# Optimization experiments

Hardware: AMD Instinct MI355X
Metric: run time of the kernel (lower is better)

Reference implementation:

```python
import jax, jax.numpy as jnp
import numpy as np

B, T, F, D, H, L, DFF, G = 4, 2048, 512, 1024, 16, 2, 4096, 16
WSCALE = 0.03  # ~1/sqrt(D) so activations stay well-conditioned


def setup_inputs() -> dict:
    key = jax.random.key(0)
    ks = iter(jax.random.split(key, 24))

    def w(shape):
        return jax.random.normal(next(ks), shape, jnp.float32) * WSCALE

    return {
        "x": jax.random.normal(next(ks), (B, T, F), jnp.float32),
        "proj_w": w((D, F)), "proj_b": jnp.zeros((D,), jnp.float32),
        "wq": w((L, D, D)), "wk": w((L, D, D)), "wv": w((L, D, D)),
        "bq": jnp.zeros((L, D), jnp.float32), "bk": jnp.zeros((L, D), jnp.float32), "bv": jnp.zeros((L, D), jnp.float32),
        "wo": w((L, D, D)), "bo": jnp.zeros((L, D), jnp.float32),
        "ln1_g": jnp.ones((L, D), jnp.float32), "ln1_b": jnp.zeros((L, D), jnp.float32),
        "ln2_g": jnp.ones((L, D), jnp.float32), "ln2_b": jnp.zeros((L, D), jnp.float32),
        "w1": w((L, DFF, D)), "b1": jnp.zeros((L, DFF), jnp.float32),
        "w2": w((L, D, DFF)), "b2": jnp.zeros((L, D), jnp.float32),
        "hw1": w((G, D, D)), "hb1": jnp.zeros((G, D), jnp.float32),
        "hw2": w((G, 2, D)), "hb2": jnp.zeros((G, 2), jnp.float32),
        "nhead": H,
    }


def _ln(x, g, b, eps=1e-5):
    m = x.mean(-1, keepdims=True)
    v = ((x - m) ** 2).mean(-1, keepdims=True)
    return (x - m) * jax.lax.rsqrt(v + eps) * g + b


def _pe(t, d):
    # sinusoidal positional encoding, shape (t, d) (d even -> sin/cos interleave)
    pos = jnp.arange(t, dtype=jnp.float32)[:, None]
    div = jnp.exp(jnp.arange(0, d, 2, dtype=jnp.float32) * (-np.log(10000.0) / d))
    ph = pos * div
    return jnp.stack([jnp.sin(ph), jnp.cos(ph)], axis=-1).reshape(t, d)


def reference(x, proj_w, proj_b, wq, wk, wv, bq, bk, bv, wo, bo,
              ln1_g, ln1_b, ln2_g, ln2_b, w1, b1, w2, b2,
              hw1, hb1, hw2, hb2, nhead):
    Bx, Tx, _ = x.shape
    Dm = proj_w.shape[0]
    dh = Dm // nhead
    h = x @ proj_w.T + proj_b + _pe(Tx, Dm)  # (B,T,D)
    for l in range(wq.shape[0]):  # post-norm encoder layers
        q = (h @ wq[l].T + bq[l]).reshape(Bx, Tx, nhead, dh)
        k = (h @ wk[l].T + bk[l]).reshape(Bx, Tx, nhead, dh)
        v = (h @ wv[l].T + bv[l]).reshape(Bx, Tx, nhead, dh)
        # explicit (non-fused) attention path, as forced by need_weights=True
        scores = jnp.einsum('bthd,bshd->bhts', q, k) / jnp.sqrt(jnp.float32(dh))
        attn = jax.nn.softmax(scores, axis=-1)  # (B,H,T,T)
        ctx = jnp.einsum('bhts,bshd->bthd', attn, v).reshape(Bx, Tx, Dm)
        h = _ln(h + ctx @ wo[l].T + bo[l], ln1_g[l], ln1_b[l])
        ff = jax.nn.relu(h @ w1[l].T + b1[l]) @ w2[l].T + b2[l]
        h = _ln(h + ff, ln2_g[l], ln2_b[l])
    hl = h[:, -1, :]  # last-token pooling, (B,D)
    z = jax.nn.relu(jnp.einsum('bd,gkd->bgk', hl, hw1) + hb1)  # per-sector hidden
    logits = jnp.einsum('bgk,gok->bgo', z, hw2) + hb2           # (B,G,2)
    return jax.nn.softmax(logits, axis=-1)
```

## Files before the change

kernel.cpp:

```cpp
#include <hip/hip_runtime.h>
#include <hip/hip_bf16.h>
#include <cstdint>
#include <cstddef>


typedef __bf16 bf16_t;
typedef __attribute__((ext_vector_type(8))) __bf16 bf16x8;
typedef __attribute__((ext_vector_type(4))) __bf16 bf16x4;
typedef __attribute__((ext_vector_type(4))) float f32x4;

#define DEV __device__ __forceinline__
#define AS1 __attribute__((address_space(1)))
#define AS3 __attribute__((address_space(3)))

DEV void gload_lds16(const void* g, void* l) {
  __builtin_amdgcn_global_load_lds((AS1 void*)(g), (AS3 void*)(l), 16, 0, 0);
}

DEV char* swz_ptr(void* base, int row, int colb) {
  return (char*)base + row * 128 + ((((colb >> 4) ^ (row & 7))) << 4) + (colb & 15);
}
DEV const char* swz_ptr(const void* base, int row, int colb) {
  return (const char*)base + row * 128 + ((((colb >> 4) ^ (row & 7))) << 4) +
         (colb & 15);
}

__global__ __launch_bounds__(256) void f2b_kernel(const float* __restrict__ s,
                                                  bf16_t* __restrict__ d, int n4) {
  const int i = blockIdx.x * 256 + threadIdx.x;
  if (i >= n4) return;
  const float4 v = *(const float4*)&s[(size_t)i * 4];
  bf16x4 o = {(bf16_t)v.x, (bf16_t)v.y, (bf16_t)v.z, (bf16_t)v.w};
  *(bf16x4*)&d[(size_t)i * 4] = o;
}

__global__ __launch_bounds__(256) void bcat_kernel(const float* __restrict__ bq,
                                                   const float* __restrict__ bk,
                                                   const float* __restrict__ bv,
                                                   float* __restrict__ out) {
  const int idx = blockIdx.x * 256 + threadIdx.x;
  const int l = idx / 3072, r = idx - l * 3072;
  const int p = r >> 10, i = r & 1023;
  const float* s = (p == 0) ? bq : ((p == 1) ? bk : bv);
  out[idx] = s[l * 1024 + i];
}

__global__ __launch_bounds__(256) void pe_kernel(float* __restrict__ pe) {
  const int idx = blockIdx.x * 256 + threadIdx.x;
  const int t = idx >> 9, i = idx & 511;
  const float dv = __expf((float)(2 * i) * -0.008994473019508785f);
  const float ph = (float)t * dv;
  pe[(size_t)t * 1024 + 2 * i] = sinf(ph);
  pe[(size_t)t * 1024 + 2 * i + 1] = cosf(ph);
}

template <int EPI>
__global__ __launch_bounds__(512, 1) void gemm8(
    const bf16_t* __restrict__ A, const bf16_t* __restrict__ W,
    const float* __restrict__ bias, bf16_t* __restrict__ outb,
    float* __restrict__ outf, const float* __restrict__ res32,
    const float* __restrict__ pe, int M, int N, int K) {
  __shared__ char smem[3][49152];
  const int tid = threadIdx.x, wv = tid >> 6, ln = tid & 63;
  const int nwg = gridDim.x * gridDim.y;
  int bid = blockIdx.y * gridDim.x + blockIdx.x;
  bid = (bid & 7) * (nwg >> 3) + (bid >> 3);
  const int m0 = (bid / gridDim.x) * 256, n0 = (bid % gridDim.x) * 128;
  const int wr = (wv >> 1) * 64, wc = (wv & 1) * 64;
  f32x4 acc[4][4] = {};

  const int tp = tid ^ ((tid >> 3) & 7);
  const int srow = tp >> 3, sc8 = (tp & 7) * 8;
  const bf16_t* pa[4];
  const bf16_t* pb[2];
#pragma unroll
  for (int u = 0; u < 4; ++u) pa[u] = A + (size_t)(m0 + u * 64 + srow) * K + sc8;
#pragma unroll
  for (int u = 0; u < 2; ++u) pb[u] = W + (size_t)(n0 + u * 64 + srow) * K + sc8;
  const int wvb = wv * 1024;

  auto stage = [&](int s) {
    char* bA = &smem[s][0] + wvb;
    char* bB = &smem[s][32768] + wvb;
#pragma unroll
    for (int u = 0; u < 4; ++u) {
      gload_lds16(pa[u], bA + u * 8192);
      pa[u] += 64;
    }
#pragma unroll
    for (int u = 0; u < 2; ++u) {
      gload_lds16(pb[u], bB + u * 8192);
      pb[u] += 64;
    }
  };

  const int NK = K >> 6;
  stage(0);
  stage(1);
  stage(2);
  asm volatile("s_waitcnt vmcnt(12)" ::: "memory");
  __builtin_amdgcn_s_barrier();

  for (int kt = 0; kt < NK; ++kt) {
    const char* bA = &smem[kt % 3][0];
    const char* bB = &smem[kt % 3][32768];
#pragma unroll
    for (int ks = 0; ks < 2; ++ks) {
      const int cb = ks * 64 + (ln >> 4) * 16;
      bf16x8 aF[4], bF[4];
#pragma unroll
      for (int m = 0; m < 4; ++m) {
        const int lb = (wr + m * 16 + (ln & 15)) * 128 + cb;
        aF[m] = *(const bf16x8*)(bA + (lb ^ (((lb >> 7) & 7) << 4)));
      }
#pragma unroll
      for (int n = 0; n < 4; ++n) {
        const int lb = (wc + n * 16 + (ln & 15)) * 128 + cb;
        bF[n] = *(const bf16x8*)(bB + (lb ^ (((lb >> 7) & 7) << 4)));
      }
      __builtin_amdgcn_s_setprio(1);
#pragma unroll
      for (int m = 0; m < 4; ++m)
#pragma unroll
        for (int n = 0; n < 4; ++n)
          acc[m][n] =
              __builtin_amdgcn_mfma_f32_16x16x32_bf16(aF[m], bF[n], acc[m][n], 0, 0, 0);
      __builtin_amdgcn_s_setprio(0);
    }
    __builtin_amdgcn_s_barrier();
    if (kt + 3 < NK) {
      stage(kt % 3);
      asm volatile("s_waitcnt vmcnt(12)" ::: "memory");
    } else if (kt + 2 < NK) {
      asm volatile("s_waitcnt vmcnt(6)" ::: "memory");
    } else {
      asm volatile("s_waitcnt vmcnt(0)" ::: "memory");
    }
    __builtin_amdgcn_s_barrier();
    __builtin_amdgcn_sched_barrier(0);
  }

  const int rr = (ln >> 4) * 4, cc = ln & 15;
#pragma unroll
  for (int m = 0; m < 4; ++m) {
    const int rowb = m0 + wr + m * 16 + rr;
#pragma unroll
    for (int n = 0; n < 4; ++n) {
      const int col = n0 + wc + n * 16 + cc;
      const float bv = bias[col];
#pragma unroll
      for (int r = 0; r < 4; ++r) {
        const int row = rowb + r;
        float v = acc[m][n][r] + bv;
        const size_t o = (size_t)row * N + col;
        if constexpr (EPI == 1) {
          v = fmaxf(v, 0.f);
          outb[o] = (bf16_t)v;
        } else if constexpr (EPI == 2) {
          v += pe[(size_t)(row & 2047) * 1024 + col];
          outb[o] = (bf16_t)v;
          outf[o] = v;
        } else if constexpr (EPI == 3) {
          v += res32[o];
          outf[o] = v;
        } else {
          outb[o] = (bf16_t)v;
        }
      }
    }
  }
}

__global__ __launch_bounds__(256) void ln_kernel(const float* __restrict__ pre,
                                                 const float* __restrict__ g,
                                                 const float* __restrict__ b,
                                                 bf16_t* __restrict__ h16,
                                                 float* __restrict__ h32) {
  const int row = blockIdx.x, tid = threadIdx.x;
  const size_t base = (size_t)row * 1024 + tid * 4;
  const float4 v = *(const float4*)&pre[base];
  float s = v.x + v.y + v.z + v.w;
  float s2 = v.x * v.x + v.y * v.y + v.z * v.z + v.w * v.w;
#pragma unroll
  for (int m = 1; m < 64; m <<= 1) {
    s += __shfl_xor(s, m);
    s2 += __shfl_xor(s2, m);
  }
  __shared__ float ls[4], ls2[4];
  if ((tid & 63) == 0) {
    ls[tid >> 6] = s;
    ls2[tid >> 6] = s2;
  }
  __syncthreads();
  s = ls[0] + ls[1] + ls[2] + ls[3];
  s2 = ls2[0] + ls2[1] + ls2[2] + ls2[3];
  const float mean = s * (1.f / 1024.f);
  const float var = s2 * (1.f / 1024.f) - mean * mean;
  const float rs = rsqrtf(var + 1e-5f);
  const float4 gv = *(const float4*)&g[tid * 4];
  const float4 bv = *(const float4*)&b[tid * 4];
  const float o0 = (v.x - mean) * rs * gv.x + bv.x;
  const float o1 = (v.y - mean) * rs * gv.y + bv.y;
  const float o2 = (v.z - mean) * rs * gv.z + bv.z;
  const float o3 = (v.w - mean) * rs * gv.w + bv.w;
  bf16x4 ob = {(bf16_t)o0, (bf16_t)o1, (bf16_t)o2, (bf16_t)o3};
  *(bf16x4*)&h16[base] = ob;
  float4 of = {o0, o1, o2, o3};
  *(float4*)&h32[base] = of;
}

__global__ __launch_bounds__(256) void transpose_v(const bf16_t* __restrict__ v,
                                                   bf16_t* __restrict__ vt) {
  __shared__ bf16_t tile[64][80];
  const int bh = blockIdx.y, t0 = blockIdx.x * 64;
  const int tid = threadIdx.x;
  const int b = bh >> 4;
  const size_t vbase = ((size_t)(b * 2048 + t0)) * 3072 + (bh & 15) * 64;
#pragma unroll
  for (int p = 0; p < 2; ++p) {
    const int chunk = p * 256 + tid;
    const int tr = chunk >> 3, c8 = (chunk & 7) * 8;
    *(bf16x8*)&tile[tr][c8] = *(const bf16x8*)&v[vbase + (size_t)tr * 3072 + c8];
  }
  __syncthreads();
  const int d = tid >> 2, t8 = (tid & 3) * 16;
  bf16_t tmp[16];
#pragma unroll
  for (int j = 0; j < 16; ++j) tmp[j] = tile[t8 + j][d];
  const size_t obase = ((size_t)bh * 64 + d) * 2048 + t0 + t8;
  *(bf16x8*)&vt[obase] = *(bf16x8*)&tmp[0];
  *(bf16x8*)&vt[obase + 8] = *(bf16x8*)&tmp[8];
}

__global__ __launch_bounds__(256, 2) void attn_kernel(const bf16_t* __restrict__ qkv,
                                                      const bf16_t* __restrict__ vt,
                                                      bf16_t* __restrict__ ctx) {
  constexpr float SCL = 0.18033688011112042f;
  constexpr int QS = 3072;
  __shared__ bf16_t lK[2][64 * 64];
  __shared__ bf16_t lV[2][64 * 64];
  __shared__ bf16_t lP[4][16 * 64];
  const int tid = threadIdx.x, wv = tid >> 6, ln = tid & 63;
  const int nwg = gridDim.x * gridDim.y;
  int bid = blockIdx.y * gridDim.x + blockIdx.x;
  bid = (bid & 7) * (nwg >> 3) + (bid >> 3);
  const int bh = bid / gridDim.x, b = bh >> 4, h = bh & 15;
  const int q0 = (bid % gridDim.x) * 64;
  const int qrow = q0 + wv * 16 + (ln & 15);
  const bf16_t* qp = qkv + (size_t)(b * 2048 + qrow) * QS + h * 64 + (ln >> 4) * 8;
  const bf16x8 aQ0 = *(const bf16x8*)qp;
  const bf16x8 aQ1 = *(const bf16x8*)(qp + 32);
  f32x4 O[4] = {};
  float m_q = -1e30f, l_q = 0.f;
  const int sr = tid >> 3;
  const int scS = ((tid & 7) ^ ((tid >> 3) & 7)) * 8;
  const bf16_t* kp0 = qkv + 1024 + (size_t)(b * 2048 + sr) * QS + h * 64 + scS;
  const bf16_t* kp1 = kp0 + (size_t)32 * QS;
  const bf16_t* vp0 = vt + (size_t)bh * 64 * 2048 + (size_t)sr * 2048 + scS;
  const bf16_t* vp1 = vp0 + 32 * 2048;

  auto stage = [&](int bufi) {
    char* dk = (char*)&lK[bufi][0] + wv * 1024;
    char* dv = (char*)&lV[bufi][0] + wv * 1024;
    gload_lds16(kp0, dk);
    gload_lds16(kp1, dk + 4096);
    gload_lds16(vp0, dv);
    gload_lds16(vp1, dv + 4096);
    kp0 += (size_t)64 * QS;
    kp1 += (size_t)64 * QS;
    vp0 += 64;
    vp1 += 64;
  };

  stage(0);
  asm volatile("s_waitcnt vmcnt(0)" ::: "memory");
  __builtin_amdgcn_s_barrier();

  for (int st = 0; st < 32; ++st) {
    const int cur = st & 1;
    if (st + 1 < 32) stage(cur ^ 1);
    f32x4 sc[4] = {};
    __builtin_amdgcn_s_setprio(1);
#pragma unroll
    for (int ks = 0; ks < 2; ++ks) {
      const int ko = ks * 32 + (ln >> 4) * 8;
      const bf16x8 aQ = ks ? aQ1 : aQ0;
#pragma unroll
      for (int nt = 0; nt < 4; ++nt) {
        const bf16x8 bK = *(const bf16x8*)swz_ptr(&lK[cur][0], nt * 16 + (ln & 15), ko * 2);
        sc[nt] = __builtin_amdgcn_mfma_f32_16x16x32_bf16(bK, aQ, sc[nt], 0, 0, 0);
      }
    }
    __builtin_amdgcn_s_setprio(0);
    float mx = fmaxf(fmaxf(sc[0][0], sc[0][1]), fmaxf(sc[0][2], sc[0][3]));
#pragma unroll
    for (int nt = 1; nt < 4; ++nt)
      mx = fmaxf(mx, fmaxf(fmaxf(sc[nt][0], sc[nt][1]), fmaxf(sc[nt][2], sc[nt][3])));
    mx *= SCL;
    mx = fmaxf(mx, __shfl_xor(mx, 16));
    mx = fmaxf(mx, __shfl_xor(mx, 32));
    if (__any(mx > m_q + 8.f)) {
      const float mnew = fmaxf(m_q, mx);
      const float alpha = exp2f(m_q - mnew);
      m_q = mnew;
      l_q *= alpha;
      float ar[4];
#pragma unroll
      for (int r = 0; r < 4; ++r) ar[r] = __shfl(alpha, (ln >> 4) * 4 + r);
#pragma unroll
      for (int dt = 0; dt < 4; ++dt)
#pragma unroll
        for (int r = 0; r < 4; ++r) O[dt][r] *= ar[r];
    }
    float rs = 0.f;
#pragma unroll
    for (int nt = 0; nt < 4; ++nt) {
      bf16x4 pb;
#pragma unroll
      for (int r = 0; r < 4; ++r) {
        const float p = exp2f(sc[nt][r] * SCL - m_q);
        rs += p;
        pb[r] = (bf16_t)p;
      }
      *(bf16x4*)swz_ptr(&lP[wv][0], ln & 15, nt * 32 + (ln >> 4) * 8) = pb;
    }
    rs += __shfl_xor(rs, 16);
    rs += __shfl_xor(rs, 32);
    l_q += rs;
    __builtin_amdgcn_s_setprio(1);
#pragma unroll
    for (int ks = 0; ks < 2; ++ks) {
      const int ko = ks * 32 + (ln >> 4) * 8;
      const bf16x8 aP = *(const bf16x8*)swz_ptr(&lP[wv][0], ln & 15, ko * 2);
#pragma unroll
      for (int dt = 0; dt < 4; ++dt) {
        const bf16x8 bV = *(const bf16x8*)swz_ptr(&lV[cur][0], dt * 16 + (ln & 15), ko * 2);
        O[dt] = __builtin_amdgcn_mfma_f32_16x16x32_bf16(aP, bV, O[dt], 0, 0, 0);
      }
    }
    __builtin_amdgcn_s_setprio(0);
    asm volatile("s_waitcnt vmcnt(0)" ::: "memory");
    __builtin_amdgcn_s_barrier();
    __builtin_amdgcn_sched_barrier(0);
  }
  const float invl = 1.f / l_q;
  float ir[4];
#pragma unroll
  for (int r = 0; r < 4; ++r) ir[r] = __shfl(invl, (ln >> 4) * 4 + r);
  const int orow = b * 2048 + q0 + wv * 16 + (ln >> 4) * 4;
#pragma unroll
  for (int r = 0; r < 4; ++r) {
#pragma unroll
    for (int dt = 0; dt < 4; ++dt)
      ctx[((size_t)(orow + r)) * 1024 + h * 64 + dt * 16 + (ln & 15)] =
          (bf16_t)(O[dt][r] * ir[r]);
  }
}

__global__ __launch_bounds__(256) void head_z(const float* __restrict__ h32,
                                              const float* __restrict__ hw1,
                                              const float* __restrict__ hb1,
                                              float* __restrict__ z) {
  const int g = blockIdx.x, slab = blockIdx.y;
  const int wv = threadIdx.x >> 6, ln = threadIdx.x & 63;
  float4 hl[4][4];
#pragma unroll
  for (int b = 0; b < 4; ++b)
#pragma unroll
    for (int c = 0; c < 4; ++c)
      hl[b][c] = *(const float4*)&h32[((size_t)b * 2048 + 2047) * 1024 + c * 256 + ln * 4];
  const int k0 = slab * 64 + wv * 16;
  for (int kk = 0; kk < 16; ++kk) {
    const int kq = k0 + kk;
    const float* wrow = hw1 + ((size_t)g * 1024 + kq) * 1024;
    float p[4] = {0, 0, 0, 0};
#pragma unroll
    for (int c = 0; c < 4; ++c) {
      const float4 w4 = *(const float4*)&wrow[c * 256 + ln * 4];
#pragma unroll
      for (int b = 0; b < 4; ++b)
        p[b] += w4.x * hl[b][c].x + w4.y * hl[b][c].y + w4.z * hl[b][c].z +
                w4.w * hl[b][c].w;
    }
#pragma unroll
    for (int m = 1; m < 64; m <<= 1)
#pragma unroll
      for (int b = 0; b < 4; ++b) p[b] += __shfl_xor(p[b], m);
    if (ln == 0) {
#pragma unroll
      for (int b = 0; b < 4; ++b)
        z[((size_t)b * 16 + g) * 1024 + kq] = fmaxf(p[b] + hb1[g * 1024 + kq], 0.f);
    }
  }
}

__global__ __launch_bounds__(64) void head_logits(const float* __restrict__ z,
                                                  const float* __restrict__ hw2,
                                                  const float* __restrict__ hb2,
                                                  float* __restrict__ out) {
  const int b = blockIdx.x, g = blockIdx.y, ln = threadIdx.x;
  const float* zr = z + ((size_t)b * 16 + g) * 1024;
  const float* w0 = hw2 + (size_t)g * 2048;
  const float* w1 = w0 + 1024;
  float p0 = 0.f, p1 = 0.f;
#pragma unroll
  for (int c = 0; c < 4; ++c) {
    const float4 zv = *(const float4*)&zr[c * 256 + ln * 4];
    const float4 a0 = *(const float4*)&w0[c * 256 + ln * 4];
    const float4 a1 = *(const float4*)&w1[c * 256 + ln * 4];
    p0 += zv.x * a0.x + zv.y * a0.y + zv.z * a0.z + zv.w * a0.w;
    p1 += zv.x * a1.x + zv.y * a1.y + zv.z * a1.z + zv.w * a1.w;
  }
#pragma unroll
  for (int m = 1; m < 64; m <<= 1) {
    p0 += __shfl_xor(p0, m);
    p1 += __shfl_xor(p1, m);
  }
  if (ln == 0) {
    const float l0 = p0 + hb2[g * 2], l1 = p1 + hb2[g * 2 + 1];
    const float mx = fmaxf(l0, l1);
    const float e0 = expf(l0 - mx), e1 = expf(l1 - mx);
    const float inv = 1.f / (e0 + e1);
    out[(size_t)b * 32 + g * 2] = e0 * inv;
    out[(size_t)b * 32 + g * 2 + 1] = e1 * inv;
  }
}

extern "C" void kernel_launch(void* const* d_in, const int* in_sizes, int n_in,
                              void* d_out, int out_size, void* d_ws, size_t ws_size,
                              hipStream_t stream) {
  const float* x = (const float*)d_in[0];
  const float* proj_w = (const float*)d_in[1];
  const float* proj_b = (const float*)d_in[2];
  const float* wq = (const float*)d_in[3];
  const float* wk = (const float*)d_in[4];
  const float* wvv = (const float*)d_in[5];
  const float* bq = (const float*)d_in[6];
  const float* bk = (const float*)d_in[7];
  const float* bv = (const float*)d_in[8];
  const float* wo = (const float*)d_in[9];
  const float* bo = (const float*)d_in[10];
  const float* ln1_g = (const float*)d_in[11];
  const float* ln1_b = (const float*)d_in[12];
  const float* ln2_g = (const float*)d_in[13];
  const float* ln2_b = (const float*)d_in[14];
  const float* w1 = (const float*)d_in[15];
  const float* b1 = (const float*)d_in[16];
  const float* w2 = (const float*)d_in[17];
  const float* b2 = (const float*)d_in[18];
  const float* hw1 = (const float*)d_in[19];
  const float* hb1 = (const float*)d_in[20];
  const float* hw2 = (const float*)d_in[21];
  const float* hb2 = (const float*)d_in[22];
  float* out = (float*)d_out;
  char* ws = (char*)d_ws;

  size_t o = 0;
  auto take = [&](size_t bytes) { size_t r = o; o += bytes; return r; };
  const size_t o_wqkv = take(12582912);
  const size_t o_wo = take(4194304);
  const size_t o_w1 = take(16777216);
  const size_t o_w2 = take(16777216);
  const size_t o_pw = take(1048576);
  const size_t o_h16 = take(16777216);
  const size_t o_h32 = take(33554432);
  const size_t o_pre = take(33554432);
  const size_t o_r4 = take(67108864);
  const size_t o_r5 = take(16777216);
  const size_t o_z = take(262144);
  const size_t o_bqkv = take(24576);

  bf16_t* wqkv16 = (bf16_t*)(ws + o_wqkv);
  bf16_t* wo16 = (bf16_t*)(ws + o_wo);
  bf16_t* w1_16 = (bf16_t*)(ws + o_w1);
  bf16_t* w2_16 = (bf16_t*)(ws + o_w2);
  bf16_t* pw16 = (bf16_t*)(ws + o_pw);
  bf16_t* h16 = (bf16_t*)(ws + o_h16);
  float* h32 = (float*)(ws + o_h32);
  float* pre32 = (float*)(ws + o_pre);
  bf16_t* qkv16 = (bf16_t*)(ws + o_r4);
  bf16_t* vT16 = (bf16_t*)(ws + o_r4 + 50331648);
  bf16_t* ff1 = (bf16_t*)(ws + o_r4);
  bf16_t* x16 = (bf16_t*)(ws + o_r5);
  float* pe32 = (float*)(ws + o_r5 + 8388608);
  bf16_t* ctx16 = (bf16_t*)(ws + o_r5);
  float* zbuf = (float*)(ws + o_z);
  float* bqkv = (float*)(ws + o_bqkv);

  f2b_kernel<<<4096, 256, 0, stream>>>(x, x16, 1048576);
  f2b_kernel<<<512, 256, 0, stream>>>(proj_w, pw16, 131072);
  for (int l = 0; l < 2; ++l) {
    f2b_kernel<<<1024, 256, 0, stream>>>(wq + (size_t)l * 1048576,
                                         wqkv16 + (size_t)(l * 3 + 0) * 1048576, 262144);
    f2b_kernel<<<1024, 256, 0, stream>>>(wk + (size_t)l * 1048576,
                                         wqkv16 + (size_t)(l * 3 + 1) * 1048576, 262144);
    f2b_kernel<<<1024, 256, 0, stream>>>(wvv + (size_t)l * 1048576,
                                         wqkv16 + (size_t)(l * 3 + 2) * 1048576, 262144);
  }
  f2b_kernel<<<2048, 256, 0, stream>>>(wo, wo16, 524288);
  f2b_kernel<<<8192, 256, 0, stream>>>(w1, w1_16, 2097152);
  f2b_kernel<<<8192, 256, 0, stream>>>(w2, w2_16, 2097152);
  bcat_kernel<<<24, 256, 0, stream>>>(bq, bk, bv, bqkv);
  pe_kernel<<<4096, 256, 0, stream>>>(pe32);

  gemm8<2><<<dim3(8, 32), 512, 0, stream>>>(x16, pw16, proj_b, h16, h32, nullptr,
                                            pe32, 8192, 1024, 512);

  for (int l = 0; l < 2; ++l) {
    const bf16_t* wqkv_l = wqkv16 + (size_t)l * 3145728;
    const bf16_t* wo_l = wo16 + (size_t)l * 1048576;
    const bf16_t* w1_l = w1_16 + (size_t)l * 4194304;
    const bf16_t* w2_l = w2_16 + (size_t)l * 4194304;

    gemm8<0><<<dim3(24, 32), 512, 0, stream>>>(h16, wqkv_l, bqkv + l * 3072, qkv16,
                                               nullptr, nullptr, nullptr, 8192, 3072,
                                               1024);
    transpose_v<<<dim3(32, 64), 256, 0, stream>>>(qkv16 + 2048, vT16);
    attn_kernel<<<dim3(32, 64), 256, 0, stream>>>(qkv16, vT16, ctx16);
    gemm8<3><<<dim3(8, 32), 512, 0, stream>>>(ctx16, wo_l, bo + l * 1024, nullptr,
                                              pre32, h32, nullptr, 8192, 1024, 1024);
    ln_kernel<<<8192, 256, 0, stream>>>(pre32, ln1_g + l * 1024, ln1_b + l * 1024, h16,
                                        h32);
    gemm8<1><<<dim3(32, 32), 512, 0, stream>>>(h16, w1_l, b1 + l * 4096, ff1, nullptr,
                                               nullptr, nullptr, 8192, 4096, 1024);
    gemm8<3><<<dim3(8, 32), 512, 0, stream>>>(ff1, w2_l, b2 + l * 1024, nullptr, pre32,
                                              h32, nullptr, 8192, 1024, 4096);
    ln_kernel<<<8192, 256, 0, stream>>>(pre32, ln2_g + l * 1024, ln2_b + l * 1024, h16,
                                        h32);
  }

  head_z<<<dim3(16, 16), 256, 0, stream>>>(h32, hw1, hb1, zbuf);
  head_logits<<<dim3(4, 16), 64, 0, stream>>>(zbuf, hw2, hb2, out);
}
```

Measured before the change: 997.1 us.

## Templatize GEMM on tile width, use 256-wide tiles and double buffering

```diff
diff --git a/kernel.cpp b/kernel.cpp
--- a/kernel.cpp
+++ b/kernel.cpp
@@ -54,29 +54,34 @@
   pe[(size_t)t * 1024 + 2 * i + 1] = cosf(ph);
 }
 
-template <int EPI>
-__global__ __launch_bounds__(512, 1) void gemm8(
+template <int EPI, int BN>
+__global__ __launch_bounds__(512, 2) void gemm9(
     const bf16_t* __restrict__ A, const bf16_t* __restrict__ W,
     const float* __restrict__ bias, bf16_t* __restrict__ outb,
     float* __restrict__ outf, const float* __restrict__ res32,
     const float* __restrict__ pe, int M, int N, int K) {
-  __shared__ char smem[3][49152];
+  constexpr int NBB = BN / 64;
+  constexpr int LPT = 4 + NBB;
+  constexpr int MF = (BN == 256) ? 8 : 4;
+  constexpr int BUFSZ = 32768 + BN * 128;
+  __shared__ char smem[2][BUFSZ];
   const int tid = threadIdx.x, wv = tid >> 6, ln = tid & 63;
   const int nwg = gridDim.x * gridDim.y;
   int bid = blockIdx.y * gridDim.x + blockIdx.x;
   bid = (bid & 7) * (nwg >> 3) + (bid >> 3);
-  const int m0 = (bid / gridDim.x) * 256, n0 = (bid % gridDim.x) * 128;
-  const int wr = (wv >> 1) * 64, wc = (wv & 1) * 64;
-  f32x4 acc[4][4] = {};
+  const int m0 = (bid / gridDim.x) * 256, n0 = (bid % gridDim.x) * BN;
+  const int wrow = (BN == 256) ? (wv >> 2) * 128 : (wv >> 1) * 64;
+  const int wcol = (BN == 256) ? (wv & 3) * 64 : (wv & 1) * 64;
+  f32x4 acc[MF][4] = {};
 
   const int tp = tid ^ ((tid >> 3) & 7);
   const int srow = tp >> 3, sc8 = (tp & 7) * 8;
   const bf16_t* pa[4];
-  const bf16_t* pb[2];
+  const bf16_t* pb[NBB];
 #pragma unroll
   for (int u = 0; u < 4; ++u) pa[u] = A + (size_t)(m0 + u * 64 + srow) * K + sc8;
 #pragma unroll
-  for (int u = 0; u < 2; ++u) pb[u] = W + (size_t)(n0 + u * 64 + srow) * K + sc8;
+  for (int u = 0; u < NBB; ++u) pb[u] = W + (size_t)(n0 + u * 64 + srow) * K + sc8;
   const int wvb = wv * 1024;
 
   auto stage = [&](int s) {
@@ -88,52 +93,60 @@
       pa[u] += 64;
     }
 #pragma unroll
-    for (int u = 0; u < 2; ++u) {
+    for (int u = 0; u < NBB; ++u) {
       gload_lds16(pb[u], bB + u * 8192);
       pb[u] += 64;
     }
+  };
+
+  auto wait_lpt = [&]() {
+    if constexpr (LPT == 8)
+      asm volatile("s_waitcnt vmcnt(8)" ::: "memory");
+    else
+      asm volatile("s_waitcnt vmcnt(6)" ::: "memory");
   };
 
   const int NK = K >> 6;
   stage(0);
   stage(1);
-  stage(2);
-  asm volatile("s_waitcnt vmcnt(12)" ::: "memory");
+  wait_lpt();
   __builtin_amdgcn_s_barrier();
 
   for (int kt = 0; kt < NK; ++kt) {
-    const char* bA = &smem[kt % 3][0];
-    const char* bB = &smem[kt % 3][32768];
+    const char* bA = &smem[kt & 1][0];
+    const char* bB = &smem[kt & 1][32768];
 #pragma unroll
     for (int ks = 0; ks < 2; ++ks) {
       const int cb = ks * 64 + (ln >> 4) * 16;
-      bf16x8 aF[4], bF[4];
-#pragma unroll
-      for (int m = 0; m < 4; ++m) {
-        const int lb = (wr + m * 16 + (ln & 15)) * 128 + cb;
-        aF[m] = *(const bf16x8*)(bA + (lb ^ (((lb >> 7) & 7) << 4)));
-      }
+      bf16x8 bF[4];
 #pragma unroll
       for (int n = 0; n < 4; ++n) {
-        const int lb = (wc + n * 16 + (ln & 15)) * 128 + cb;
+        const int lb = (wcol + n * 16 + (ln & 15)) * 128 + cb;
         bF[n] = *(const bf16x8*)(bB + (lb ^ (((lb >> 7) & 7) << 4)));
       }
-      __builtin_amdgcn_s_setprio(1);
-#pragma unroll
-      for (int m = 0; m < 4; ++m)
-#pragma unroll
-        for (int n = 0; n < 4; ++n)
-          acc[m][n] =
-              __builtin_amdgcn_mfma_f32_16x16x32_bf16(aF[m], bF[n], acc[m][n], 0, 0, 0);
-      __builtin_amdgcn_s_setprio(0);
+#pragma unroll
+      for (int mh = 0; mh < 2; ++mh) {
+        bf16x8 aF[MF / 2];
+#pragma unroll
+        for (int m = 0; m < MF / 2; ++m) {
+          const int lb = (wrow + (mh * (MF / 2) + m) * 16 + (ln & 15)) * 128 + cb;
+          aF[m] = *(const bf16x8*)(bA + (lb ^ (((lb >> 7) & 7) << 4)));
+        }
+        __builtin_amdgcn_s_setprio(1);
+#pragma unroll
+        for (int m = 0; m < MF / 2; ++m)
+#pragma unroll
+          for (int n = 0; n < 4; ++n)
+            acc[mh * (MF / 2) + m][n] = __builtin_amdgcn_mfma_f32_16x16x32_bf16(
+                aF[m], bF[n], acc[mh * (MF / 2) + m][n], 0, 0, 0);
+        __builtin_amdgcn_s_setprio(0);
+      }
     }
     __builtin_amdgcn_s_barrier();
-    if (kt + 3 < NK) {
-      stage(kt % 3);
-      asm volatile("s_waitcnt vmcnt(12)" ::: "memory");
-    } else if (kt + 2 < NK) {
-      asm volatile("s_waitcnt vmcnt(6)" ::: "memory");
-    } else {
+    if (kt + 2 < NK) {
+      stage(kt & 1);
+      wait_lpt();
+    } else if (kt + 1 < NK) {
       asm volatile("s_waitcnt vmcnt(0)" ::: "memory");
     }
     __builtin_amdgcn_s_barrier();
@@ -142,11 +155,11 @@
 
   const int rr = (ln >> 4) * 4, cc = ln & 15;
 #pragma unroll
-  for (int m = 0; m < 4; ++m) {
-    const int rowb = m0 + wr + m * 16 + rr;
+  for (int m = 0; m < MF; ++m) {
+    const int rowb = m0 + wrow + m * 16 + rr;
 #pragma unroll
     for (int n = 0; n < 4; ++n) {
-      const int col = n0 + wc + n * 16 + cc;
+      const int col = n0 + wcol + n * 16 + cc;
       const float bv = bias[col];
 #pragma unroll
       for (int r = 0; r < 4; ++r) {
@@ -232,7 +245,7 @@
   *(bf16x8*)&vt[obase + 8] = *(bf16x8*)&tmp[8];
 }
 
-__global__ __launch_bounds__(256, 2) void attn_kernel(const bf16_t* __restrict__ qkv,
+__global__ __launch_bounds__(256, 4) void attn_kernel(const bf16_t* __restrict__ qkv,
                                                       const bf16_t* __restrict__ vt,
                                                       bf16_t* __restrict__ ctx) {
   constexpr float SCL = 0.18033688011112042f;
@@ -503,8 +516,8 @@
   bcat_kernel<<<24, 256, 0, stream>>>(bq, bk, bv, bqkv);
   pe_kernel<<<4096, 256, 0, stream>>>(pe32);
 
-  gemm8<2><<<dim3(8, 32), 512, 0, stream>>>(x16, pw16, proj_b, h16, h32, nullptr,
-                                            pe32, 8192, 1024, 512);
+  gemm9<2, 128><<<dim3(8, 32), 512, 0, stream>>>(x16, pw16, proj_b, h16, h32, nullptr,
+                                                 pe32, 8192, 1024, 512);
 
   for (int l = 0; l < 2; ++l) {
     const bf16_t* wqkv_l = wqkv16 + (size_t)l * 3145728;
@@ -512,19 +525,22 @@
     const bf16_t* w1_l = w1_16 + (size_t)l * 4194304;
     const bf16_t* w2_l = w2_16 + (size_t)l * 4194304;
 
-    gemm8<0><<<dim3(24, 32), 512, 0, stream>>>(h16, wqkv_l, bqkv + l * 3072, qkv16,
-                                               nullptr, nullptr, nullptr, 8192, 3072,
-                                               1024);
+    gemm9<0, 256><<<dim3(12, 32), 512, 0, stream>>>(h16, wqkv_l, bqkv + l * 3072, qkv16,
+                                                    nullptr, nullptr, nullptr, 8192,
+                                                    3072, 1024);
     transpose_v<<<dim3(32, 64), 256, 0, stream>>>(qkv16 + 2048, vT16);
     attn_kernel<<<dim3(32, 64), 256, 0, stream>>>(qkv16, vT16, ctx16);
-    gemm8<3><<<dim3(8, 32), 512, 0, stream>>>(ctx16, wo_l, bo + l * 1024, nullptr,
-                                              pre32, h32, nullptr, 8192, 1024, 1024);
+    gemm9<3, 128><<<dim3(8, 32), 512, 0, stream>>>(ctx16, wo_l, bo + l * 1024, nullptr,
+                                                   pre32, h32, nullptr, 8192, 1024,
+                                                   1024);
     ln_kernel<<<8192, 256, 0, stream>>>(pre32, ln1_g + l * 1024, ln1_b + l * 1024, h16,
                                         h32);
-    gemm8<1><<<dim3(32, 32), 512, 0, stream>>>(h16, w1_l, b1 + l * 4096, ff1, nullptr,
-                                               nullptr, nullptr, 8192, 4096, 1024);
-    gemm8<3><<<dim3(8, 32), 512, 0, stream>>>(ff1, w2_l, b2 + l * 1024, nullptr, pre32,
-                                              h32, nullptr, 8192, 1024, 4096);
+    gemm9<1, 256><<<dim3(16, 32), 512, 0, stream>>>(h16, w1_l, b1 + l * 4096, ff1,
+                                                    nullptr, nullptr, nullptr, 8192,
+                                                    4096, 1024);
+    gemm9<3, 128><<<dim3(8, 32), 512, 0, stream>>>(ff1, w2_l, b2 + l * 1024, nullptr,
+                                                   pre32, h32, nullptr, 8192, 1024,
+                                                   4096);
     ln_kernel<<<8192, 256, 0, stream>>>(pre32, ln2_g + l * 1024, ln2_b + l * 1024, h16,
                                         h32);
   }
```

Measured after the change: 954.2 us. 1.04x faster.
